# Performance work log

Measured on AMD Instinct MI355X. Metric: run time of the kernel, lower is better.

The kernel has to match this reference:

```python
import jax, jax.numpy as jnp
import numpy as np

D_MODEL = 1024
NUM_HEADS = 16
D_K = D_MODEL // NUM_HEADS


def setup_inputs() -> dict:
    key = jax.random.key(0)
    kq, kk, kv, k1, k2, k3, k4 = jax.random.split(key, 7)
    B, S = 2, 2048
    # Xavier-uniform init for square [d_model, d_model] weights
    limit = float(np.sqrt(6.0 / (D_MODEL + D_MODEL)))
    def xav(k):
        return jax.random.uniform(k, (D_MODEL, D_MODEL), jnp.float32, -limit, limit)
    return {
        "query": jax.random.normal(kq, (B, S, D_MODEL), jnp.float32),
        "key": jax.random.normal(kk, (B, S, D_MODEL), jnp.float32),
        "value": jax.random.normal(kv, (B, S, D_MODEL), jnp.float32),
        "W_q": xav(k1),
        "W_k": xav(k2),
        "W_v": xav(k3),
        "W_o": xav(k4),
    }


def reference(query, key, value, W_q, W_k, W_v, W_o):
    B, Sq, _ = query.shape
    Sk = key.shape[1]
    # Linear layers: y = x @ W.T (torch nn.Linear convention)
    Q = (query @ W_q.T).reshape(B, Sq, NUM_HEADS, D_K).transpose(0, 2, 1, 3)
    K = (key @ W_k.T).reshape(B, Sk, NUM_HEADS, D_K).transpose(0, 2, 1, 3)
    V = (value @ W_v.T).reshape(B, Sk, NUM_HEADS, D_K).transpose(0, 2, 1, 3)
    scale = 1.0 / jnp.sqrt(jnp.asarray(D_K, Q.dtype))
    scores = jnp.einsum("bhqd,bhkd->bhqk", Q, K) * scale  # [B,H,Sq,Sk]
    attn = jax.nn.softmax(scores, axis=-1)
    # dropout is identity in eval mode
    out = jnp.einsum("bhqk,bhkd->bhqd", attn, V)
    out = out.transpose(0, 2, 1, 3).reshape(B, Sq, D_MODEL)
    return out @ W_o.T
```

## Files before the change

kernel.cpp:

```cpp
#include <hip/hip_runtime.h>
#include <math.h>

typedef unsigned short ushort_t;
typedef __attribute__((ext_vector_type(8))) short short8;
typedef __attribute__((ext_vector_type(4))) float f32x4;
typedef __attribute__((ext_vector_type(4))) unsigned short ushort4v;
typedef __attribute__((ext_vector_type(2))) unsigned int uint2v;

#define D_MODEL 1024
#define SEQ 2048
#define MROWS 4096
#define PLANE (MROWS * D_MODEL)
#define WELEM (D_MODEL * D_MODEL)

static __device__ __forceinline__ ushort_t f2bf(float f) {
    unsigned u = __builtin_bit_cast(unsigned, f);
    return (ushort_t)((u + 0x7fffu + ((u >> 16) & 1u)) >> 16);
}
static __device__ __forceinline__ unsigned cvtpk(float lo, float hi) {
    unsigned r;
    asm("v_cvt_pk_bf16_f32 %0, %1, %2" : "=v"(r) : "v"(lo), "v"(hi));
    return r;
}

#define GLDS16(gp, lp)                                                         \
    __builtin_amdgcn_global_load_lds(                                          \
        (const __attribute__((address_space(1))) void*)(gp),                   \
        (__attribute__((address_space(3))) void*)(lp), 16, 0, 0)

__global__ __launch_bounds__(256)
void cvt_all(const float* __restrict__ q, const float* __restrict__ k,
             const float* __restrict__ v, const float* __restrict__ w0,
             const float* __restrict__ w1, const float* __restrict__ w2,
             const float* __restrict__ w3, ushort_t* __restrict__ dst) {
    int blk = blockIdx.x;
    const float* s;
    size_t base;
    if (blk < 6144) {
        const int p = blk >> 11;
        s = (p == 0) ? q : (p == 1) ? k : v;
        base = (size_t)p * PLANE;
        blk &= 2047;
    } else {
        const int p = (blk - 6144) >> 9;
        s = (p == 0) ? w0 : (p == 1) ? w1 : (p == 2) ? w2 : w3;
        base = 3 * (size_t)PLANE + (size_t)p * WELEM;
        blk = (blk - 6144) & 511;
    }
    const int i = (blk * 256 + threadIdx.x) * 8;
    float4 a = *(const float4*)(s + i);
    float4 bb = *(const float4*)(s + i + 4);
    short8 o;
    o[0] = (short)f2bf(a.x); o[1] = (short)f2bf(a.y);
    o[2] = (short)f2bf(a.z); o[3] = (short)f2bf(a.w);
    o[4] = (short)f2bf(bb.x); o[5] = (short)f2bf(bb.y);
    o[6] = (short)f2bf(bb.z); o[7] = (short)f2bf(bb.w);
    *(short8*)(dst + base + i) = o;
}

__global__ __launch_bounds__(256)
void gemm3(const ushort_t* __restrict__ Xq, const ushort_t* __restrict__ Wb,
           ushort_t* __restrict__ Cb) {
    __shared__ __align__(16) ushort_t As[128 * 64];
    __shared__ __align__(16) ushort_t Bs[128 * 64];

    const int z = blockIdx.z;
    const ushort_t* A = Xq + (size_t)z * PLANE;
    const ushort_t* B = Wb + (size_t)z * WELEM;
    ushort_t* C = Cb + (size_t)z * PLANE;

    const int tid = threadIdx.x;
    const int lane = tid & 63;
    const int wid = tid >> 6;
    const int wr = wid >> 1, wc = wid & 1;
    const int brow = blockIdx.y * 128;
    const int bcol = blockIdx.x * 128;

    const int lrow = lane >> 3;
    const int loff = ((lane & 7) ^ lrow) * 8;

    const ushort_t* aS[4];
    const ushort_t* bS[4];
#pragma unroll
    for (int i = 0; i < 4; ++i) {
        aS[i] = A + (size_t)(brow + wid * 32 + i * 8 + lrow) * D_MODEL + loff;
        bS[i] = B + (size_t)(bcol + wid * 32 + i * 8 + lrow) * D_MODEL + loff;
    }

    f32x4 acc[4][4];
#pragma unroll
    for (int i = 0; i < 4; ++i)
#pragma unroll
        for (int j = 0; j < 4; ++j) acc[i][j] = {0.f, 0.f, 0.f, 0.f};

    const int fr = lane & 15, fg = lane >> 4;

    for (int k0 = 0; k0 < D_MODEL; k0 += 64) {
        __syncthreads();
#pragma unroll
        for (int i = 0; i < 4; ++i) {
            GLDS16(aS[i] + k0, As + (wid * 32 + i * 8) * 64);
            GLDS16(bS[i] + k0, Bs + (wid * 32 + i * 8) * 64);
        }
        __syncthreads();
#pragma unroll
        for (int ks = 0; ks < 2; ++ks) {
            const int coff = (ks * 32 + fg * 8) ^ ((fr & 7) << 3);
            short8 af[4], bw[4];
#pragma unroll
            for (int mi = 0; mi < 4; ++mi)
                af[mi] = *(const short8*)&As[(wr * 64 + mi * 16 + fr) * 64 + coff];
#pragma unroll
            for (int nj = 0; nj < 4; ++nj)
                bw[nj] = *(const short8*)&Bs[(wc * 64 + nj * 16 + fr) * 64 + coff];
#pragma unroll
            for (int mi = 0; mi < 4; ++mi)
#pragma unroll
                for (int nj = 0; nj < 4; ++nj)
                    acc[mi][nj] = __builtin_amdgcn_mfma_f32_16x16x32_bf16(
                        af[mi], bw[nj], acc[mi][nj], 0, 0, 0);
        }
    }

    if (z < 2) {
#pragma unroll
        for (int mi = 0; mi < 4; ++mi)
#pragma unroll
            for (int nj = 0; nj < 4; ++nj) {
                const int n = bcol + wc * 64 + nj * 16 + fr;
#pragma unroll
                for (int r = 0; r < 4; ++r) {
                    const int m = brow + wr * 64 + mi * 16 + fg * 4 + r;
                    C[(size_t)m * D_MODEL + n] = f2bf(acc[mi][nj][r]);
                }
            }
    } else {
#pragma unroll
        for (int mi = 0; mi < 4; ++mi)
#pragma unroll
            for (int nj = 0; nj < 4; ++nj) {
                const int n = bcol + wc * 64 + nj * 16 + fr;
                const int m0 = brow + wr * 64 + mi * 16 + fg * 4;
                ushort4v o4;
#pragma unroll
                for (int r = 0; r < 4; ++r) o4[r] = f2bf(acc[mi][nj][r]);
                *(ushort4v*)&C[((size_t)(m0 >> 11) << 21) + (size_t)n * SEQ + (m0 & 2047)] = o4;
            }
    }
}

__global__ __launch_bounds__(256)
void gemm_out(const ushort_t* __restrict__ A, const ushort_t* __restrict__ B,
              float* __restrict__ C) {
    __shared__ __align__(16) ushort_t As[2][128 * 64];
    __shared__ __align__(16) ushort_t Bs[2][64 * 64];

    const int tid = threadIdx.x;
    const int lane = tid & 63;
    const int wid = tid >> 6;
    const int wr = wid >> 1, wc = wid & 1;
    const int brow = blockIdx.y * 128;
    const int bcol = blockIdx.x * 64;

    const int lrow = lane >> 3;
    const int loff = ((lane & 7) ^ lrow) * 8;

    const ushort_t* aSrc[4];
    const ushort_t* bSrc[2];
#pragma unroll
    for (int i = 0; i < 4; ++i)
        aSrc[i] = A + (size_t)(brow + (wid * 4 + i) * 8 + lrow) * D_MODEL + loff;
#pragma unroll
    for (int i = 0; i < 2; ++i)
        bSrc[i] = B + (size_t)(bcol + (wid * 2 + i) * 8 + lrow) * D_MODEL + loff;

    f32x4 acc[4][2];
#pragma unroll
    for (int i = 0; i < 4; ++i)
#pragma unroll
        for (int j = 0; j < 2; ++j) acc[i][j] = {0.f, 0.f, 0.f, 0.f};

    const int fr = lane & 15, fg = lane >> 4;

#pragma unroll
    for (int i = 0; i < 4; ++i) GLDS16(aSrc[i], As[0] + (wid * 4 + i) * 512);
#pragma unroll
    for (int i = 0; i < 2; ++i) GLDS16(bSrc[i], Bs[0] + (wid * 2 + i) * 512);

    int cur = 0;
    for (int k0 = 0; k0 < D_MODEL; k0 += 64) {
        __syncthreads();
        if (k0 + 64 < D_MODEL) {
#pragma unroll
            for (int i = 0; i < 4; ++i)
                GLDS16(aSrc[i] + k0 + 64, As[cur ^ 1] + (wid * 4 + i) * 512);
#pragma unroll
            for (int i = 0; i < 2; ++i)
                GLDS16(bSrc[i] + k0 + 64, Bs[cur ^ 1] + (wid * 2 + i) * 512);
        }
#pragma unroll
        for (int ks = 0; ks < 2; ++ks) {
            const int coff = (ks * 32 + fg * 8) ^ ((fr & 7) << 3);
            short8 af[4], bw[2];
#pragma unroll
            for (int mi = 0; mi < 4; ++mi)
                af[mi] = *(const short8*)&As[cur][(wr * 64 + mi * 16 + fr) * 64 + coff];
#pragma unroll
            for (int nj = 0; nj < 2; ++nj)
                bw[nj] = *(const short8*)&Bs[cur][(wc * 32 + nj * 16 + fr) * 64 + coff];
#pragma unroll
            for (int mi = 0; mi < 4; ++mi)
#pragma unroll
                for (int nj = 0; nj < 2; ++nj)
                    acc[mi][nj] = __builtin_amdgcn_mfma_f32_16x16x32_bf16(
                        af[mi], bw[nj], acc[mi][nj], 0, 0, 0);
        }
        cur ^= 1;
    }

#pragma unroll
    for (int mi = 0; mi < 4; ++mi)
#pragma unroll
        for (int nj = 0; nj < 2; ++nj) {
            const int n = bcol + wc * 32 + nj * 16 + fr;
#pragma unroll
            for (int r = 0; r < 4; ++r) {
                const int m = brow + wr * 64 + mi * 16 + fg * 4 + r;
                C[(size_t)m * D_MODEL + n] = acc[mi][nj][r];
            }
        }
}

__global__ __launch_bounds__(256)
void attn_mfma(const ushort_t* __restrict__ Qp, const ushort_t* __restrict__ Kp,
               const ushort_t* __restrict__ VT, ushort_t* __restrict__ Ap) {
    __shared__ __align__(16) ushort_t Ks[2][64 * 64];
    __shared__ __align__(16) ushort_t Vs[2][64 * 64];
    __shared__ __align__(16) ushort_t Ps[4 * 32 * 64];

    const int tid = threadIdx.x;
    const int lane = tid & 63;
    const int wid = tid >> 6;
    const int bid = blockIdx.x;
    const int qt = bid & 15;
    const int h = (bid >> 4) & 15;
    const int b = bid >> 8;

    const int lrow = lane >> 3;
    const int loff = ((lane & 7) ^ lrow) * 8;
    const int fr = lane & 15, fg = lane >> 4;

    const int m0 = b * SEQ + qt * 128;

#pragma unroll
    for (int j = 0; j < 4; ++j) {
        const ushort_t* qS =
            Qp + (size_t)(m0 + wid * 32 + j * 8 + lrow) * D_MODEL + h * 64 + loff;
        GLDS16(qS, Ps + (wid * 32 + j * 8) * 64);
    }
    const ushort_t* kS[2];
    const ushort_t* vS[2];
#pragma unroll
    for (int j = 0; j < 2; ++j) {
        const int cr = (wid * 2 + j) * 8 + lrow;
        kS[j] = Kp + (size_t)(b * SEQ + cr) * D_MODEL + h * 64 + loff;
        vS[j] = VT + ((size_t)b << 21) + (size_t)(h * 64 + cr) * SEQ + loff;
        GLDS16(kS[j], Ks[0] + (wid * 2 + j) * 512);
        GLDS16(vS[j], Vs[0] + (wid * 2 + j) * 512);
        kS[j] += 64 * D_MODEL;
        vS[j] += 64;
    }
    __syncthreads();

    short8 aq[2][2];
#pragma unroll
    for (int qh = 0; qh < 2; ++qh)
#pragma unroll
        for (int ks = 0; ks < 2; ++ks)
            aq[qh][ks] = *(const short8*)&Ps[(wid * 32 + qh * 16 + fr) * 64 +
                                             ((ks * 32 + fg * 8) ^ ((fr & 7) << 3))];

    f32x4 accO[2][4];
#pragma unroll
    for (int qh = 0; qh < 2; ++qh)
#pragma unroll
        for (int nd = 0; nd < 4; ++nd) accO[qh][nd] = {0.f, 0.f, 0.f, 0.f};
    float m_s[2] = {-INFINITY, -INFINITY};
    float l_p[2] = {0.f, 0.f};

    const float CEXP = 0.18033688011112042f;

    int cur = 0;
    for (int kt = 0; kt < SEQ / 64; ++kt) {
        __syncthreads();
        if (kt + 1 < SEQ / 64) {
#pragma unroll
            for (int j = 0; j < 2; ++j) {
                GLDS16(kS[j], Ks[cur ^ 1] + (wid * 2 + j) * 512);
                GLDS16(vS[j], Vs[cur ^ 1] + (wid * 2 + j) * 512);
                kS[j] += 64 * D_MODEL;
                vS[j] += 64;
            }
        }

        f32x4 accS[2][4];
#pragma unroll
        for (int qh = 0; qh < 2; ++qh)
#pragma unroll
            for (int n = 0; n < 4; ++n) accS[qh][n] = {0.f, 0.f, 0.f, 0.f};
#pragma unroll
        for (int ks = 0; ks < 2; ++ks) {
            const int coff = (ks * 32 + fg * 8) ^ ((fr & 7) << 3);
            short8 ak[4];
#pragma unroll
            for (int n = 0; n < 4; ++n)
                ak[n] = *(const short8*)&Ks[cur][(n * 16 + fr) * 64 + coff];
#pragma unroll
            for (int qh = 0; qh < 2; ++qh)
#pragma unroll
                for (int n = 0; n < 4; ++n)
                    accS[qh][n] = __builtin_amdgcn_mfma_f32_16x16x32_bf16(
                        ak[n], aq[qh][ks], accS[qh][n], 0, 0, 0);
        }

#pragma unroll
        for (int qh = 0; qh < 2; ++qh) {
            float mx = accS[qh][0][0];
#pragma unroll
            for (int n = 0; n < 4; ++n)
#pragma unroll
                for (int r = 0; r < 4; ++r) mx = fmaxf(mx, accS[qh][n][r]);
            mx = fmaxf(mx, __shfl_xor(mx, 16));
            mx = fmaxf(mx, __shfl_xor(mx, 32));
            const float cand = mx * CEXP;
            if (__any(cand > m_s[qh] + 8.f)) {
                const float mnew = fmaxf(m_s[qh], cand);
                const float al = __builtin_amdgcn_exp2f(m_s[qh] - mnew);
                m_s[qh] = mnew;
                l_p[qh] *= al;
#pragma unroll
                for (int r = 0; r < 4; ++r) {
                    const float ar = __shfl(al, (lane & 48) | (fg * 4 + r));
#pragma unroll
                    for (int nd = 0; nd < 4; ++nd) accO[qh][nd][r] *= ar;
                }
            }
            float ps = 0.f;
            const float nm = -m_s[qh];
#pragma unroll
            for (int n = 0; n < 4; ++n)
#pragma unroll
                for (int r = 0; r < 4; ++r) {
                    const float p = __builtin_amdgcn_exp2f(fmaf(accS[qh][n][r], CEXP, nm));
                    accS[qh][n][r] = p;
                    ps += p;
                }
            l_p[qh] += ps;

            const int pbase = wid * 2048 + (qh * 16 + fr) * 64;
#pragma unroll
            for (int n = 0; n < 4; ++n) {
                uint2v pw2 = {cvtpk(accS[qh][n][0], accS[qh][n][1]),
                              cvtpk(accS[qh][n][2], accS[qh][n][3])};
                const int w = (n * 4 + fg) ^ (fr & 14);
                *(uint2v*)&Ps[pbase + w * 4] = pw2;
            }
        }

#pragma unroll
        for (int ks = 0; ks < 2; ++ks) {
            const int coff = (ks * 32 + fg * 8) ^ ((fr & 7) << 3);
            short8 bv[4];
#pragma unroll
            for (int nd = 0; nd < 4; ++nd)
                bv[nd] = *(const short8*)&Vs[cur][(nd * 16 + fr) * 64 + coff];
#pragma unroll
            for (int qh = 0; qh < 2; ++qh) {
                const int p0 = (ks * 8 + 2 * fg) ^ (fr & 14);
                short8 ap = *(const short8*)&Ps[wid * 2048 + (qh * 16 + fr) * 64 + p0 * 4];
#pragma unroll
                for (int nd = 0; nd < 4; ++nd)
                    accO[qh][nd] = __builtin_amdgcn_mfma_f32_16x16x32_bf16(
                        ap, bv[nd], accO[qh][nd], 0, 0, 0);
            }
        }
        cur ^= 1;
    }

#pragma unroll
    for (int qh = 0; qh < 2; ++qh) {
        float lt = l_p[qh];
        lt += __shfl_xor(lt, 16);
        lt += __shfl_xor(lt, 32);
#pragma unroll
        for (int r = 0; r < 4; ++r) {
            const float lq = __shfl(lt, (lane & 48) | (fg * 4 + r));
            const float inv = 1.0f / lq;
            const int row = m0 + wid * 32 + qh * 16 + fg * 4 + r;
#pragma unroll
            for (int nd = 0; nd < 4; ++nd)
                Ap[(size_t)row * D_MODEL + h * 64 + nd * 16 + fr] =
                    f2bf(accO[qh][nd][r] * inv);
        }
    }
}

extern "C" void kernel_launch(void* const* d_in, const int* in_sizes, int n_in,
                              void* d_out, int out_size, void* d_ws, size_t ws_size,
                              hipStream_t stream) {
    const float* query = (const float*)d_in[0];
    const float* key   = (const float*)d_in[1];
    const float* value = (const float*)d_in[2];
    const float* W_q   = (const float*)d_in[3];
    const float* W_k   = (const float*)d_in[4];
    const float* W_v   = (const float*)d_in[5];
    const float* W_o   = (const float*)d_in[6];
    float* out = (float*)d_out;

    ushort_t* ws = (ushort_t*)d_ws;
    ushort_t* Xq = ws;
    ushort_t* Wb = ws + 3 * (size_t)PLANE;
    ushort_t* Qp = ws + 4 * (size_t)PLANE;
    ushort_t* Kp = Qp + (size_t)PLANE;
    ushort_t* VT = Kp + (size_t)PLANE;
    ushort_t* Ap = VT + (size_t)PLANE;

    cvt_all<<<8192, 256, 0, stream>>>(query, key, value, W_q, W_k, W_v, W_o, Xq);

    dim3 g3(D_MODEL / 128, MROWS / 128, 3);
    gemm3<<<g3, 256, 0, stream>>>(Xq, Wb, Qp);

    attn_mfma<<<512, 256, 0, stream>>>(Qp, Kp, VT, Ap);

    dim3 go(D_MODEL / 64, MROWS / 128);
    gemm_out<<<go, 256, 0, stream>>>(Ap, Wb + 3 * (size_t)WELEM, out);
}
```

Before: 140.9 us.

## Split attention work across 8 waves of 16 query rows with MFMA priority hints

```diff
diff --git a/kernel.cpp b/kernel.cpp
--- a/kernel.cpp
+++ b/kernel.cpp
@@ -231,12 +231,12 @@
         }
 }
 
-__global__ __launch_bounds__(256)
+__global__ __launch_bounds__(512)
 void attn_mfma(const ushort_t* __restrict__ Qp, const ushort_t* __restrict__ Kp,
                const ushort_t* __restrict__ VT, ushort_t* __restrict__ Ap) {
     __shared__ __align__(16) ushort_t Ks[2][64 * 64];
     __shared__ __align__(16) ushort_t Vs[2][64 * 64];
-    __shared__ __align__(16) ushort_t Ps[4 * 32 * 64];
+    __shared__ __align__(16) ushort_t Ps[8 * 16 * 64];
 
     const int tid = threadIdx.x;
     const int lane = tid & 63;
@@ -253,155 +253,131 @@
     const int m0 = b * SEQ + qt * 128;
 
 #pragma unroll
-    for (int j = 0; j < 4; ++j) {
+    for (int j = 0; j < 2; ++j) {
         const ushort_t* qS =
-            Qp + (size_t)(m0 + wid * 32 + j * 8 + lrow) * D_MODEL + h * 64 + loff;
-        GLDS16(qS, Ps + (wid * 32 + j * 8) * 64);
-    }
-    const ushort_t* kS[2];
-    const ushort_t* vS[2];
-#pragma unroll
-    for (int j = 0; j < 2; ++j) {
-        const int cr = (wid * 2 + j) * 8 + lrow;
-        kS[j] = Kp + (size_t)(b * SEQ + cr) * D_MODEL + h * 64 + loff;
-        vS[j] = VT + ((size_t)b << 21) + (size_t)(h * 64 + cr) * SEQ + loff;
-        GLDS16(kS[j], Ks[0] + (wid * 2 + j) * 512);
-        GLDS16(vS[j], Vs[0] + (wid * 2 + j) * 512);
-        kS[j] += 64 * D_MODEL;
-        vS[j] += 64;
-    }
+            Qp + (size_t)(m0 + wid * 16 + j * 8 + lrow) * D_MODEL + h * 64 + loff;
+        GLDS16(qS, Ps + (wid * 16 + j * 8) * 64);
+    }
+    const ushort_t* kS =
+        Kp + (size_t)(b * SEQ + wid * 8 + lrow) * D_MODEL + h * 64 + loff;
+    const ushort_t* vS =
+        VT + ((size_t)b << 21) + (size_t)(h * 64 + wid * 8 + lrow) * SEQ + loff;
+    GLDS16(kS, Ks[0] + wid * 512);
+    GLDS16(vS, Vs[0] + wid * 512);
+    kS += 64 * D_MODEL;
+    vS += 64;
     __syncthreads();
 
-    short8 aq[2][2];
-#pragma unroll
-    for (int qh = 0; qh < 2; ++qh)
-#pragma unroll
-        for (int ks = 0; ks < 2; ++ks)
-            aq[qh][ks] = *(const short8*)&Ps[(wid * 32 + qh * 16 + fr) * 64 +
-                                             ((ks * 32 + fg * 8) ^ ((fr & 7) << 3))];
-
-    f32x4 accO[2][4];
-#pragma unroll
-    for (int qh = 0; qh < 2; ++qh)
-#pragma unroll
-        for (int nd = 0; nd < 4; ++nd) accO[qh][nd] = {0.f, 0.f, 0.f, 0.f};
-    float m_s[2] = {-INFINITY, -INFINITY};
-    float l_p[2] = {0.f, 0.f};
+    short8 aq[2];
+#pragma unroll
+    for (int ks = 0; ks < 2; ++ks)
+        aq[ks] = *(const short8*)&Ps[(wid * 16 + fr) * 64 +
+                                     ((ks * 32 + fg * 8) ^ ((fr & 7) << 3))];
+
+    f32x4 accO[4];
+#pragma unroll
+    for (int nd = 0; nd < 4; ++nd) accO[nd] = {0.f, 0.f, 0.f, 0.f};
+    float m_s = -INFINITY;
+    float l_p = 0.f;
 
     const float CEXP = 0.18033688011112042f;
+    const int pbase = wid * 1024 + fr * 64;
 
     int cur = 0;
     for (int kt = 0; kt < SEQ / 64; ++kt) {
         __syncthreads();
         if (kt + 1 < SEQ / 64) {
-#pragma unroll
-            for (int j = 0; j < 2; ++j) {
-                GLDS16(kS[j], Ks[cur ^ 1] + (wid * 2 + j) * 512);
-                GLDS16(vS[j], Vs[cur ^ 1] + (wid * 2 + j) * 512);
-                kS[j] += 64 * D_MODEL;
-                vS[j] += 64;
-            }
-        }
-
-        f32x4 accS[2][4];
-#pragma unroll
-        for (int qh = 0; qh < 2; ++qh)
-#pragma unroll
-            for (int n = 0; n < 4; ++n) accS[qh][n] = {0.f, 0.f, 0.f, 0.f};
+            GLDS16(kS, Ks[cur ^ 1] + wid * 512);
+            GLDS16(vS, Vs[cur ^ 1] + wid * 512);
+            kS += 64 * D_MODEL;
+            vS += 64;
+        }
+
+        f32x4 accS[4];
+#pragma unroll
+        for (int n = 0; n < 4; ++n) accS[n] = {0.f, 0.f, 0.f, 0.f};
+        __builtin_amdgcn_s_setprio(1);
 #pragma unroll
         for (int ks = 0; ks < 2; ++ks) {
             const int coff = (ks * 32 + fg * 8) ^ ((fr & 7) << 3);
-            short8 ak[4];
-#pragma unroll
-            for (int n = 0; n < 4; ++n)
-                ak[n] = *(const short8*)&Ks[cur][(n * 16 + fr) * 64 + coff];
-#pragma unroll
-            for (int qh = 0; qh < 2; ++qh)
-#pragma unroll
-                for (int n = 0; n < 4; ++n)
-                    accS[qh][n] = __builtin_amdgcn_mfma_f32_16x16x32_bf16(
-                        ak[n], aq[qh][ks], accS[qh][n], 0, 0, 0);
-        }
-
-#pragma unroll
-        for (int qh = 0; qh < 2; ++qh) {
-            float mx = accS[qh][0][0];
-#pragma unroll
-            for (int n = 0; n < 4; ++n)
-#pragma unroll
-                for (int r = 0; r < 4; ++r) mx = fmaxf(mx, accS[qh][n][r]);
-            mx = fmaxf(mx, __shfl_xor(mx, 16));
-            mx = fmaxf(mx, __shfl_xor(mx, 32));
-            const float cand = mx * CEXP;
-            if (__any(cand > m_s[qh] + 8.f)) {
-                const float mnew = fmaxf(m_s[qh], cand);
-                const float al = __builtin_amdgcn_exp2f(m_s[qh] - mnew);
-                m_s[qh] = mnew;
-                l_p[qh] *= al;
-#pragma unroll
-                for (int r = 0; r < 4; ++r) {
-                    const float ar = __shfl(al, (lane & 48) | (fg * 4 + r));
-#pragma unroll
-                    for (int nd = 0; nd < 4; ++nd) accO[qh][nd][r] *= ar;
-                }
-            }
-            float ps = 0.f;
-            const float nm = -m_s[qh];
-#pragma unroll
-            for (int n = 0; n < 4; ++n)
-#pragma unroll
-                for (int r = 0; r < 4; ++r) {
-                    const float p = __builtin_amdgcn_exp2f(fmaf(accS[qh][n][r], CEXP, nm));
-                    accS[qh][n][r] = p;
-                    ps += p;
-                }
-            l_p[qh] += ps;
-
-            const int pbase = wid * 2048 + (qh * 16 + fr) * 64;
 #pragma unroll
             for (int n = 0; n < 4; ++n) {
-                uint2v pw2 = {cvtpk(accS[qh][n][0], accS[qh][n][1]),
-                              cvtpk(accS[qh][n][2], accS[qh][n][3])};
-                const int w = (n * 4 + fg) ^ (fr & 14);
-                *(uint2v*)&Ps[pbase + w * 4] = pw2;
-            }
-        }
-
+                short8 ak = *(const short8*)&Ks[cur][(n * 16 + fr) * 64 + coff];
+                accS[n] = __builtin_amdgcn_mfma_f32_16x16x32_bf16(ak, aq[ks],
+                                                                  accS[n], 0, 0, 0);
+            }
+        }
+        __builtin_amdgcn_s_setprio(0);
+
+        float mx = accS[0][0];
+#pragma unroll
+        for (int n = 0; n < 4; ++n)
+#pragma unroll
+            for (int r = 0; r < 4; ++r) mx = fmaxf(mx, accS[n][r]);
+        mx = fmaxf(mx, __shfl_xor(mx, 16));
+        mx = fmaxf(mx, __shfl_xor(mx, 32));
+        const float cand = mx * CEXP;
+        if (__any(cand > m_s + 8.f)) {
+            const float mnew = fmaxf(m_s, cand);
+            const float al = __builtin_amdgcn_exp2f(m_s - mnew);
+            m_s = mnew;
+            l_p *= al;
+#pragma unroll
+            for (int r = 0; r < 4; ++r) {
+                const float ar = __shfl(al, (lane & 48) | (fg * 4 + r));
+#pragma unroll
+                for (int nd = 0; nd < 4; ++nd) accO[nd][r] *= ar;
+            }
+        }
+        float ps = 0.f;
+        const float nm = -m_s;
+#pragma unroll
+        for (int n = 0; n < 4; ++n)
+#pragma unroll
+            for (int r = 0; r < 4; ++r) {
+                const float p = __builtin_amdgcn_exp2f(fmaf(accS[n][r], CEXP, nm));
+                accS[n][r] = p;
+                ps += p;
+            }
+        l_p += ps;
+
+#pragma unroll
+        for (int n = 0; n < 4; ++n) {
+            uint2v pw2 = {cvtpk(accS[n][0], accS[n][1]),
+                          cvtpk(accS[n][2], accS[n][3])};
+            const int w = (n * 4 + fg) ^ (fr & 14);
+            *(uint2v*)&Ps[pbase + w * 4] = pw2;
+        }
+
+        __builtin_amdgcn_s_setprio(1);
 #pragma unroll
         for (int ks = 0; ks < 2; ++ks) {
             const int coff = (ks * 32 + fg * 8) ^ ((fr & 7) << 3);
-            short8 bv[4];
-#pragma unroll
-            for (int nd = 0; nd < 4; ++nd)
-                bv[nd] = *(const short8*)&Vs[cur][(nd * 16 + fr) * 64 + coff];
-#pragma unroll
-            for (int qh = 0; qh < 2; ++qh) {
-                const int p0 = (ks * 8 + 2 * fg) ^ (fr & 14);
-                short8 ap = *(const short8*)&Ps[wid * 2048 + (qh * 16 + fr) * 64 + p0 * 4];
-#pragma unroll
-                for (int nd = 0; nd < 4; ++nd)
-                    accO[qh][nd] = __builtin_amdgcn_mfma_f32_16x16x32_bf16(
-                        ap, bv[nd], accO[qh][nd], 0, 0, 0);
-            }
-        }
+            const int p0 = (ks * 8 + 2 * fg) ^ (fr & 14);
+            short8 ap = *(const short8*)&Ps[pbase + p0 * 4];
+#pragma unroll
+            for (int nd = 0; nd < 4; ++nd) {
+                short8 bv = *(const short8*)&Vs[cur][(nd * 16 + fr) * 64 + coff];
+                accO[nd] = __builtin_amdgcn_mfma_f32_16x16x32_bf16(ap, bv,
+                                                                   accO[nd], 0, 0, 0);
+            }
+        }
+        __builtin_amdgcn_s_setprio(0);
         cur ^= 1;
     }
 
-#pragma unroll
-    for (int qh = 0; qh < 2; ++qh) {
-        float lt = l_p[qh];
-        lt += __shfl_xor(lt, 16);
-        lt += __shfl_xor(lt, 32);
-#pragma unroll
-        for (int r = 0; r < 4; ++r) {
-            const float lq = __shfl(lt, (lane & 48) | (fg * 4 + r));
-            const float inv = 1.0f / lq;
-            const int row = m0 + wid * 32 + qh * 16 + fg * 4 + r;
-#pragma unroll
-            for (int nd = 0; nd < 4; ++nd)
-                Ap[(size_t)row * D_MODEL + h * 64 + nd * 16 + fr] =
-                    f2bf(accO[qh][nd][r] * inv);
-        }
+    float lt = l_p;
+    lt += __shfl_xor(lt, 16);
+    lt += __shfl_xor(lt, 32);
+#pragma unroll
+    for (int r = 0; r < 4; ++r) {
+        const float lq = __shfl(lt, (lane & 48) | (fg * 4 + r));
+        const float inv = 1.0f / lq;
+        const int row = m0 + wid * 16 + fg * 4 + r;
+#pragma unroll
+        for (int nd = 0; nd < 4; ++nd)
+            Ap[(size_t)row * D_MODEL + h * 64 + nd * 16 + fr] =
+                f2bf(accO[nd][r] * inv);
     }
 }
 
@@ -430,7 +406,7 @@
     dim3 g3(D_MODEL / 128, MROWS / 128, 3);
     gemm3<<<g3, 256, 0, stream>>>(Xq, Wb, Qp);
 
-    attn_mfma<<<512, 256, 0, stream>>>(Qp, Kp, VT, Ap);
+    attn_mfma<<<512, 512, 0, stream>>>(Qp, Kp, VT, Ap);
 
     dim3 go(D_MODEL / 64, MROWS / 128);
     gemm_out<<<go, 256, 0, stream>>>(Ap, Wb + 3 * (size_t)WELEM, out);
```

Result: faster. 137.0 us (-2.8%).
